# Kernel tuning notes

Measured on AMD Instinct MI355X. Metric: run time of the kernel, lower is better.

Reference implementation:

```python
import jax, jax.numpy as jnp
import numpy as np
from jax.scipy.special import logsumexp

NEG = -1e30  # log-zero surrogate (avoids inf arithmetic)
DEN_SCALE = 1.0


def setup_inputs() -> dict:
    key = jax.random.key(0)
    k1, k2_, k3, k4 = jax.random.split(key, 4)
    B, T, C, L = 64, 2000, 256, 128
    nnet_output = jax.random.normal(k1, (B, T, C), dtype=jnp.float32)
    trans = jax.random.normal(k2_, (C, C), dtype=jnp.float32) * 0.1
    labels = jax.random.randint(k3, (B, L), 0, C, dtype=jnp.int32)
    # durations >= 1024 so the length-L numerator chain is always reachable
    durations = (1024 + jax.random.randint(k4, (B,), 0, T - 1024)).astype(jnp.int32)
    return {"nnet_output": nnet_output, "trans": trans, "labels": labels,
            "durations": durations}


def _lfmmi_scores(nnet_output, trans, labels, durations):
    """Log-semiring forward DP: numerator (linear label chain w/ self-loops)
    and denominator (dense bigram FSA over all symbols). Returns per-utt
    num - den_scale * den, as in num_tot_scores - den_scale*den_tot_scores."""
    B, T, C = nnet_output.shape
    L = labels.shape[1]
    x = jnp.moveaxis(nnet_output, 1, 0)            # [T, B, C]

    # ---- numerator: alpha over label positions [B, L] ----
    emit0 = jnp.take_along_axis(x[0], labels, axis=1)      # [B, L]
    alpha0 = jnp.full((B, L), NEG, x.dtype).at[:, 0].set(emit0[:, 0])

    def num_step(alpha, tx):
        t, x_t = tx
        emit = jnp.take_along_axis(x_t, labels, axis=1)     # [B, L]
        shifted = jnp.concatenate(
            [jnp.full((B, 1), NEG, alpha.dtype), alpha[:, :-1]], axis=1)
        new = jnp.logaddexp(alpha, shifted) + emit          # self-loop | advance
        active = (t < durations)[:, None]
        return jnp.where(active, new, alpha), None

    ts = jnp.arange(1, T)
    alpha, _ = jax.lax.scan(num_step, alpha0, (ts, x[1:]))
    num_score = alpha[:, -1]                                # [B]

    # ---- denominator: beta over symbols [B, C], dense bigram transitions ----
    beta0 = x[0]

    def den_step(beta, tx):
        t, x_t = tx
        # [B, C_prev, 1] + [1, C_prev, C_next] -> logsumexp over prev
        new = logsumexp(beta[:, :, None] + trans[None, :, :], axis=1) + x_t
        active = (t < durations)[:, None]
        return jnp.where(active, new, beta), None

    beta, _ = jax.lax.scan(den_step, beta0, (ts, x[1:]))
    den_score = logsumexp(beta, axis=1)                     # [B]

    return num_score - DEN_SCALE * den_score


def reference(nnet_output, trans, labels, durations):
    tot_scores = _lfmmi_scores(nnet_output, trans, labels, durations)  # [B]
    tot_frames = jnp.sum(durations)
    # get_tot_objf_and_num_frames: sum of (finite) per-utt scores, frame counts
    tot_score = jnp.sum(tot_scores)
    return tot_score, tot_frames, tot_frames
```

## Files before the change

### kernel.cpp

```cpp
#include <hip/hip_runtime.h>

#define NEGV -1e30f
constexpr int Bn = 64, Tn = 2000, Cn = 256, Ln = 128;

__device__ __forceinline__ float wave_max(float v) {
#pragma unroll
  for (int s = 32; s; s >>= 1) v = fmaxf(v, __shfl_xor(v, s, 64));
  return v;
}
__device__ __forceinline__ float wave_sum(float v) {
#pragma unroll
  for (int s = 32; s; s >>= 1) v += __shfl_xor(v, s, 64);
  return v;
}
__device__ __forceinline__ unsigned int bf16_rne(float f) {
  return (__float_as_uint(f) + 0x8000u) >> 16;
}

__global__ __launch_bounds__(512, 1) void lfmmi_main(
    const float* __restrict__ nnet, const float* __restrict__ trans,
    const int* __restrict__ labels, const int* __restrict__ durs,
    float* __restrict__ den_out, float* __restrict__ num_out) {
  __shared__ __align__(16) unsigned short p_bf[2][Cn];
  __shared__ __align__(16) float fin[Cn];
  __shared__ float m_lds[2];
  const int tid = threadIdx.x;
  const int blk = blockIdx.x;

  if (blk < Bn) {
    const int b = blk;
    const int dur = durs[b];
    const int w = tid >> 6;
    const int lane = tid & 63;
    const int c = lane & 31;
    const int h = lane >> 5;
    const int j = w * 32 + c;

    unsigned int Ep[64];
#pragma unroll
    for (int k = 0; k < 64; ++k) {
      const int i0 = 128 * h + 2 * k;
      const unsigned int lo = bf16_rne(__expf(trans[i0 * Cn + j]));
      const unsigned int hi = bf16_rne(__expf(trans[(i0 + 1) * Cn + j]));
      Ep[k] = (lo & 0xffffu) | (hi << 16);
    }

    const float* xb = nnet + (size_t)b * Tn * Cn;
    float beta = xb[j];
    const float m0 = xb[0];
    float m_add = m0;
    if (h == 0) p_bf[1][j] = (unsigned short)bf16_rne(__expf(beta - m0));
    if (tid == 0) m_lds[0] = m0;
    float xn1 = xb[Cn + j];
    float xn2 = xb[2 * Cn + j];
    __syncthreads();

    for (int t = 1; t < dur; ++t) {
      const int cur = t & 1;
      const float mn = m_lds[(t - 1) & 1];

      const uint4* ps = (const uint4*)&p_bf[cur][128 * h];
      float a0 = 0.f, a1 = 0.f, a2 = 0.f, a3 = 0.f;
#pragma unroll
      for (int k = 0; k < 16; ++k) {
        const uint4 q = ps[k];
        asm("v_dot2_f32_bf16 %0, %1, %2, %0" : "+v"(a0) : "v"(q.x), "v"(Ep[4 * k + 0]));
        asm("v_dot2_f32_bf16 %0, %1, %2, %0" : "+v"(a1) : "v"(q.y), "v"(Ep[4 * k + 1]));
        asm("v_dot2_f32_bf16 %0, %1, %2, %0" : "+v"(a2) : "v"(q.z), "v"(Ep[4 * k + 2]));
        asm("v_dot2_f32_bf16 %0, %1, %2, %0" : "+v"(a3) : "v"(q.w), "v"(Ep[4 * k + 3]));
      }
      float s = (a0 + a1) + (a2 + a3);
      s += __shfl_xor(s, 32, 64);
      beta = m_add + __logf(s) + xn1;

      xn1 = xn2;
      const int tn = (t + 2 < Tn) ? t + 2 : Tn - 1;
      xn2 = xb[(size_t)tn * Cn + j];

      if (h == 0)
        p_bf[cur ^ 1][j] = (unsigned short)bf16_rne(__expf(beta - mn));
      if (tid == 0) m_lds[t & 1] = beta;
      m_add = mn;
      __syncthreads();
    }

    if (h == 0) fin[j] = beta;
    __syncthreads();
    if (tid < 64) {
      const float4 v = ((const float4*)fin)[tid];
      float mx = fmaxf(fmaxf(v.x, v.y), fmaxf(v.z, v.w));
      mx = wave_max(mx);
      float sm = __expf(v.x - mx) + __expf(v.y - mx) +
                 __expf(v.z - mx) + __expf(v.w - mx);
      sm = wave_sum(sm);
      if (tid == 0) den_out[b] = mx + __logf(sm);
    }
  } else {
    const int b = blk - Bn;
    if (tid >= 64) return;
    const int dur = durs[b];
    const int lane = tid;
    const float* xb = nnet + (size_t)b * Tn * Cn;
    const int lab0 = labels[b * Ln + lane];
    const int lab1 = labels[b * Ln + 64 + lane];
    float a0 = (lane == 0) ? xb[lab0] : NEGV;
    float a1 = NEGV;
    float ea1 = xb[(size_t)1 * Cn + lab0], eb1 = xb[(size_t)1 * Cn + lab1];
    float ea2 = xb[(size_t)2 * Cn + lab0], eb2 = xb[(size_t)2 * Cn + lab1];
    float ea3 = xb[(size_t)3 * Cn + lab0], eb3 = xb[(size_t)3 * Cn + lab1];
    float ea4 = xb[(size_t)4 * Cn + lab0], eb4 = xb[(size_t)4 * Cn + lab1];

    for (int t = 1; t < dur; ++t) {
      const float ec0 = ea1, ec1 = eb1;
      ea1 = ea2; ea2 = ea3; ea3 = ea4;
      eb1 = eb2; eb2 = eb3; eb3 = eb4;
      const int tn = (t + 4 < Tn) ? t + 4 : Tn - 1;
      ea4 = xb[(size_t)tn * Cn + lab0];
      eb4 = xb[(size_t)tn * Cn + lab1];

      const float p0s = __shfl_up(a0, 1, 64);
      const float p1s = __shfl_up(a1, 1, 64);
      const float w63 = __shfl(a0, 63, 64);
      const float prev0 = lane ? p0s : NEGV;
      const float prev1 = lane ? p1s : w63;

      const float mx0 = fmaxf(a0, prev0), d0 = fminf(a0, prev0) - mx0;
      const float mx1 = fmaxf(a1, prev1), d1 = fminf(a1, prev1) - mx1;
      a0 = mx0 + log1pf(__expf(d0)) + ec0;
      a1 = mx1 + log1pf(__expf(d1)) + ec1;
    }
    if (lane == 63) num_out[b] = a1;
  }
}

__global__ void lfmmi_final(const float* __restrict__ den,
                            const float* __restrict__ num,
                            const int* __restrict__ durs,
                            float* __restrict__ out) {
  const int tid = threadIdx.x;
  float v = num[tid] - den[tid];
  float d = (float)durs[tid];
  v = wave_sum(v);
  d = wave_sum(d);
  if (tid == 0) {
    out[0] = v;
    out[1] = d;
    out[2] = d;
  }
}

extern "C" void kernel_launch(void* const* d_in, const int* in_sizes, int n_in,
                              void* d_out, int out_size, void* d_ws, size_t ws_size,
                              hipStream_t stream) {
  const float* nnet = (const float*)d_in[0];
  const float* trans = (const float*)d_in[1];
  const int* labels = (const int*)d_in[2];
  const int* durs = (const int*)d_in[3];
  float* den_ws = (float*)d_ws;
  float* num_ws = den_ws + Bn;
  lfmmi_main<<<dim3(2 * Bn), dim3(512), 0, stream>>>(nnet, trans, labels, durs,
                                                     den_ws, num_ws);
  lfmmi_final<<<dim3(1), dim3(64), 0, stream>>>(den_ws, num_ws, durs,
                                                (float*)d_out);
}
```

Baseline: 1.288 ms.

## Retile denominator matvec so each lane reuses LDS vector across four outputs

Changes the per-wave work split in the denominator recurrence. Before, each lane handled one output column over half of the previous states. Now each lane handles four output columns over a 32-state slice, so every LDS-loaded bf16 pair feeds four dot2 instructions. This cuts LDS reads per step by about 4x. In exchange the cross-lane reduction grows to three butterfly stages on four accumulators, and only half the lanes do the log/exp epilogue.

```diff
diff --git a/kernel.cpp b/kernel.cpp
--- a/kernel.cpp
+++ b/kernel.cpp
@@ -32,59 +32,73 @@
     const int dur = durs[b];
     const int w = tid >> 6;
     const int lane = tid & 63;
-    const int c = lane & 31;
-    const int h = lane >> 5;
-    const int j = w * 32 + c;
+    const int g = lane >> 3;
+    const int c = lane & 7;
+    const int gm = g & 3;
+    const int j0 = 32 * w + c + 8 * gm;
 
-    unsigned int Ep[64];
+    unsigned int Ep[16][4];
 #pragma unroll
-    for (int k = 0; k < 64; ++k) {
-      const int i0 = 128 * h + 2 * k;
-      const unsigned int lo = bf16_rne(__expf(trans[i0 * Cn + j]));
-      const unsigned int hi = bf16_rne(__expf(trans[(i0 + 1) * Cn + j]));
-      Ep[k] = (lo & 0xffffu) | (hi << 16);
+    for (int p = 0; p < 16; ++p) {
+#pragma unroll
+      for (int k = 0; k < 4; ++k) {
+        const int i0 = 32 * g + 2 * p;
+        const int j = 32 * w + c + 8 * k;
+        const unsigned int lo = bf16_rne(__expf(trans[i0 * Cn + j]));
+        const unsigned int hi = bf16_rne(__expf(trans[(i0 + 1) * Cn + j]));
+        Ep[p][k] = (lo & 0xffffu) | (hi << 16);
+      }
     }
 
     const float* xb = nnet + (size_t)b * Tn * Cn;
-    float beta = xb[j];
+    float beta = xb[j0];
     const float m0 = xb[0];
     float m_add = m0;
-    if (h == 0) p_bf[1][j] = (unsigned short)bf16_rne(__expf(beta - m0));
+    if (g < 4) p_bf[1][j0] = (unsigned short)bf16_rne(__expf(beta - m0));
     if (tid == 0) m_lds[0] = m0;
-    float xn1 = xb[Cn + j];
-    float xn2 = xb[2 * Cn + j];
+    float xn1 = xb[Cn + j0];
+    float xn2 = xb[2 * Cn + j0];
     __syncthreads();
 
     for (int t = 1; t < dur; ++t) {
       const int cur = t & 1;
       const float mn = m_lds[(t - 1) & 1];
 
-      const uint4* ps = (const uint4*)&p_bf[cur][128 * h];
+      union { uint4 q[4]; unsigned int u[16]; } P;
+      const uint4* ps = (const uint4*)&p_bf[cur][32 * g];
+      P.q[0] = ps[0]; P.q[1] = ps[1]; P.q[2] = ps[2]; P.q[3] = ps[3];
+
       float a0 = 0.f, a1 = 0.f, a2 = 0.f, a3 = 0.f;
 #pragma unroll
-      for (int k = 0; k < 16; ++k) {
-        const uint4 q = ps[k];
-        asm("v_dot2_f32_bf16 %0, %1, %2, %0" : "+v"(a0) : "v"(q.x), "v"(Ep[4 * k + 0]));
-        asm("v_dot2_f32_bf16 %0, %1, %2, %0" : "+v"(a1) : "v"(q.y), "v"(Ep[4 * k + 1]));
-        asm("v_dot2_f32_bf16 %0, %1, %2, %0" : "+v"(a2) : "v"(q.z), "v"(Ep[4 * k + 2]));
-        asm("v_dot2_f32_bf16 %0, %1, %2, %0" : "+v"(a3) : "v"(q.w), "v"(Ep[4 * k + 3]));
+      for (int p = 0; p < 16; ++p) {
+        asm("v_dot2_f32_bf16 %0, %1, %2, %0" : "+v"(a0) : "v"(P.u[p]), "v"(Ep[p][0]));
+        asm("v_dot2_f32_bf16 %0, %1, %2, %0" : "+v"(a1) : "v"(P.u[p]), "v"(Ep[p][1]));
+        asm("v_dot2_f32_bf16 %0, %1, %2, %0" : "+v"(a2) : "v"(P.u[p]), "v"(Ep[p][2]));
+        asm("v_dot2_f32_bf16 %0, %1, %2, %0" : "+v"(a3) : "v"(P.u[p]), "v"(Ep[p][3]));
       }
-      float s = (a0 + a1) + (a2 + a3);
-      s += __shfl_xor(s, 32, 64);
-      beta = m_add + __logf(s) + xn1;
+#pragma unroll
+      for (int s = 8; s <= 32; s <<= 1) {
+        a0 += __shfl_xor(a0, s, 64);
+        a1 += __shfl_xor(a1, s, 64);
+        a2 += __shfl_xor(a2, s, 64);
+        a3 += __shfl_xor(a3, s, 64);
+      }
 
-      xn1 = xn2;
-      const int tn = (t + 2 < Tn) ? t + 2 : Tn - 1;
-      xn2 = xb[(size_t)tn * Cn + j];
-
-      if (h == 0)
-        p_bf[cur ^ 1][j] = (unsigned short)bf16_rne(__expf(beta - mn));
-      if (tid == 0) m_lds[t & 1] = beta;
+      if (g < 4) {
+        const float sv = (gm & 2) ? ((gm & 1) ? a3 : a2)
+                                  : ((gm & 1) ? a1 : a0);
+        beta = m_add + __logf(sv) + xn1;
+        xn1 = xn2;
+        const int tn = (t + 2 < Tn) ? t + 2 : Tn - 1;
+        xn2 = xb[(size_t)tn * Cn + j0];
+        p_bf[cur ^ 1][j0] = (unsigned short)bf16_rne(__expf(beta - mn));
+        if (tid == 0) m_lds[t & 1] = beta;
+      }
       m_add = mn;
       __syncthreads();
     }
 
-    if (h == 0) fin[j] = beta;
+    if (g < 4) fin[j0] = beta;
     __syncthreads();
     if (tid < 64) {
       const float4 v = ((const float4*)fin)[tid];
```

New measurement: 1.576 ms. 22.4% more time.
